# Optimization experiments

Hardware: AMD Instinct MI355X
Metric: run time of the kernel (lower is better)

Reference implementation:

```python
import jax, jax.numpy as jnp
from jax import lax
import numpy as np

B, T, IN, H, L, C = 1024, 64, 64, 512, 8, 128


def setup_inputs() -> dict:
    key = jax.random.key(0)
    ks = jax.random.split(key, 11)
    s_in = 1.0 / np.sqrt(H)
    return {
        "x": jax.random.normal(ks[0], (B, T, IN), jnp.float32),
        "w_ih0": jax.random.normal(ks[1], (4 * H, IN), jnp.float32) * s_in,
        "w_hh0": jax.random.normal(ks[2], (4 * H, H), jnp.float32) * s_in,
        "b_ih0": jax.random.normal(ks[3], (4 * H,), jnp.float32) * s_in,
        "b_hh0": jax.random.normal(ks[4], (4 * H,), jnp.float32) * s_in,
        "w_ih": jax.random.normal(ks[5], (L - 1, 4 * H, H), jnp.float32) * s_in,
        "w_hh": jax.random.normal(ks[6], (L - 1, 4 * H, H), jnp.float32) * s_in,
        "b_ih": jax.random.normal(ks[7], (L - 1, 4 * H), jnp.float32) * s_in,
        "b_hh": jax.random.normal(ks[8], (L - 1, 4 * H), jnp.float32) * s_in,
        "fc_w": jax.random.normal(ks[9], (C, H * T), jnp.float32) * (1.0 / np.sqrt(H * T)),
        "fc_b": jax.random.normal(ks[10], (C,), jnp.float32) * 0.01,
    }


def _lstm_layer(x_tbd, wi, wh, bi, bh):
    # x_tbd: [T, B, D_in]; returns hidden sequence [T, B, H]
    b = x_tbd.shape[1]
    h_dim = wh.shape[1]
    bias = bi + bh

    def step(carry, x_t):
        h, c = carry
        gates = x_t @ wi.T + h @ wh.T + bias  # [B, 4H]
        i, f, g, o = jnp.split(gates, 4, axis=-1)  # PyTorch gate order i,f,g,o
        i = jax.nn.sigmoid(i)
        f = jax.nn.sigmoid(f)
        g = jnp.tanh(g)
        o = jax.nn.sigmoid(o)
        c = f * c + i * g
        h = o * jnp.tanh(c)
        return (h, c), h

    h0 = jnp.zeros((b, h_dim), x_tbd.dtype)
    _, hs = lax.scan(step, (h0, h0), x_tbd)
    return hs


def reference(x, w_ih0, w_hh0, b_ih0, b_hh0, w_ih, w_hh, b_ih, b_hh, fc_w, fc_b):
    xt = jnp.transpose(x, (1, 0, 2))  # [T, B, IN]
    h = _lstm_layer(xt, w_ih0, w_hh0, b_ih0, b_hh0)
    for l in range(w_ih.shape[0]):  # fixed small layer count
        h = _lstm_layer(h, w_ih[l], w_hh[l], b_ih[l], b_hh[l])
    out = jnp.transpose(h, (1, 0, 2)).reshape(x.shape[0], -1)  # [B, T*H]
    return out @ fc_w.T + fc_b
```

## Files before the change

kernel.cpp:

```cpp
#include <hip/hip_runtime.h>
#include <hip/hip_bf16.h>

#define BB   1024
#define TT   64
#define IND  64
#define HH   512
#define G4   2048
#define NLAYER 8
#define NCLS 128
#define KP   1024
#define RS   8
#define SLOT (32 * 1024 * 16)

typedef __bf16 bf16x8 __attribute__((ext_vector_type(8)));
typedef float  f32x4  __attribute__((ext_vector_type(4)));

typedef const __attribute__((address_space(1))) void* as1cvp;
typedef __attribute__((address_space(3))) void* as3vp;

__device__ __forceinline__ void gload16(void* lds, const void* g) {
  __builtin_amdgcn_global_load_lds((as1cvp)g, (as3vp)lds, 16, 0, 0);
}

__device__ __forceinline__ float sigmf(float x) { return 1.f / (1.f + __expf(-x)); }
__device__ __forceinline__ float tanhfast(float x) { return 2.f / (1.f + __expf(-2.f * x)) - 1.f; }

__global__ void cvt_kernel(const float* __restrict__ s, __bf16* __restrict__ d, int n) {
  int i = blockIdx.x * 256 + threadIdx.x;
  if (i < n) d[i] = (__bf16)s[i];
}

__global__ void pack_w(const float* __restrict__ whh0, const float* __restrict__ wih0,
                       const float* __restrict__ whh, const float* __restrict__ wih,
                       __bf16* __restrict__ Wp) {
  int i = blockIdx.x * 256 + threadIdx.x;
  int k = i & (KP - 1), n = (i >> 10) & 2047, l = i >> 21;
  float v;
  if (k < 512) v = (l == 0) ? whh0[n * 512 + k] : whh[((size_t)(l - 1) * G4 + n) * 512 + k];
  else if (l == 0) v = (k < 512 + IND) ? wih0[n * IND + (k - 512)] : 0.f;
  else v = wih[((size_t)(l - 1) * G4 + n) * 512 + (k - 512)];
  Wp[i] = (__bf16)v;
}

__global__ void bias_prep(const float* __restrict__ bi0, const float* __restrict__ bh0,
                          const float* __restrict__ bi, const float* __restrict__ bh,
                          float* __restrict__ biasb) {
  int i = blockIdx.x * 256 + threadIdx.x;
  int l = i >> 11, k = i & 2047;
  float v = (l == 0) ? (bi0[k] + bh0[k]) : (bi[(l - 1) * G4 + k] + bh[(l - 1) * G4 + k]);
  biasb[i] = v;
}

__global__ void zero_u32(unsigned* __restrict__ p, int n) {
  int i = blockIdx.x * 256 + threadIdx.x;
  if (i < n) p[i] = 0u;
}

__global__ __launch_bounds__(256, 2) void lstm_all(
    const float* __restrict__ xf,
    const __bf16* __restrict__ Wp,
    const float* __restrict__ biasb,
    __bf16* __restrict__ hring,
    __bf16* __restrict__ h7,
    unsigned* __restrict__ flags,
    unsigned* __restrict__ xslot) {
  extern __shared__ __bf16 Wlds[];
  __shared__ int sbs;
  const int tid = threadIdx.x;

  if (tid == 0) {
    unsigned xcc;
    asm volatile("s_getreg_b32 %0, hwreg(HW_REG_XCC_ID)" : "=s"(xcc));
    xcc &= 7u;
    unsigned slot = __hip_atomic_fetch_add(xslot + xcc, 1u, __ATOMIC_RELAXED,
                                           __HIP_MEMORY_SCOPE_AGENT) & 63u;
    sbs = (int)((xcc << 6) | slot);
  }
  __syncthreads();
  const int l  = sbs >> 6;
  const int bx = (sbs >> 5) & 1;
  const int by = sbs & 31;
  const int j0 = by << 4;
  const __bf16* Wl = Wp + (size_t)l * G4 * KP;

  for (int it = 0; it < 16; ++it) {
    const int p = it * 256 + tid;
    const int kt = p >> 8;
    const int q = p & 255;
    const int u = q >> 2;
    const int g = (q & 3) ^ ((u >> 1) & 3);
    const int n = ((u >> 4) << 9) + j0 + (u & 15);
    gload16(&Wlds[p * 8], Wl + (size_t)n * KP + kt * 32 + g * 8);
  }

  const int lane = tid & 63, wv = tid >> 6;
  const int qr = lane >> 4, ml = lane & 15;
  const __bf16* wb[4];
  float bv[4];
  int wsw[4];
#pragma unroll
  for (int g = 0; g < 4; ++g) {
    const int n = g * 512 + j0 + ml;
    wb[g] = Wl + (size_t)n * KP + 512 + qr * 8;
    bv[g] = biasb[l * G4 + n];
    const int u = g * 16 + ml;
    wsw[g] = u * 32 + ((qr ^ ((u >> 1) & 3)) << 3);
  }
  const int r0 = (bx << 9) + (wv << 7);
  const int rowA = r0 + ml;
  const int abase = ((qr >> 1) << 14) + rowA * 16 + ((qr & 1) << 3);
  __bf16* ringL = hring + (size_t)l * RS * SLOT;
  const __bf16* ringU = hring + (size_t)((l > 0 ? l : 1) - 1) * RS * SLOT;
  unsigned* ownf = flags + (l * 2 + bx) * 64;
  unsigned* upf  = flags + ((l > 0 ? l - 1 : 0) * 2 + bx) * 64;
  unsigned* dnf  = flags + ((l < 7 ? l + 1 : 7) * 2 + bx) * 64;
  float c8[8][4] = {};
  f32x4 acc[8][4];
  __syncthreads();

  auto initAcc = [&]() {
#pragma unroll
    for (int m = 0; m < 8; ++m)
#pragma unroll
      for (int g = 0; g < 4; ++g)
#pragma unroll
        for (int r = 0; r < 4; ++r) acc[m][g][r] = bv[g];
  };

  auto xpartL0 = [&](int tx) {
#pragma unroll
    for (int m = 0; m < 8; ++m) {
      const float* xr = xf + ((size_t)(rowA + m * 16) * TT + tx) * IND + qr * 8;
      const f32x4 f0 = *(const f32x4*)xr;
      const f32x4 f1 = *(const f32x4*)(xr + 4);
      const f32x4 f2 = *(const f32x4*)(xr + 32);
      const f32x4 f3 = *(const f32x4*)(xr + 36);
      bf16x8 a0, a1;
#pragma unroll
      for (int r = 0; r < 4; ++r) {
        a0[r] = (__bf16)f0[r]; a0[4 + r] = (__bf16)f1[r];
        a1[r] = (__bf16)f2[r]; a1[4 + r] = (__bf16)f3[r];
      }
#pragma unroll
      for (int g = 0; g < 4; ++g) {
        acc[m][g] = __builtin_amdgcn_mfma_f32_16x16x32_bf16(
            a0, *(const bf16x8*)(wb[g]), acc[m][g], 0, 0, 0);
        acc[m][g] = __builtin_amdgcn_mfma_f32_16x16x32_bf16(
            a1, *(const bf16x8*)(wb[g] + 32), acc[m][g], 0, 0, 0);
      }
    }
  };

  auto xpartL = [&](int tx) {
    const __bf16* src = ringU + (size_t)(tx & (RS - 1)) * SLOT + abase;
    bf16x8 A0[4], A1[4], Wr[2][4];
#pragma unroll
    for (int m = 0; m < 4; ++m) A0[m] = *(const bf16x8*)(src + m * 256);
#pragma unroll
    for (int m = 0; m < 4; ++m) A1[m] = *(const bf16x8*)(src + (4 + m) * 256);
#pragma unroll
    for (int g = 0; g < 4; ++g) Wr[0][g] = *(const bf16x8*)(wb[g]);
#pragma unroll
    for (int kt = 0; kt < 16; ++kt) {
      const __bf16* aknx = src + (kt + 1) * 32768;
#pragma unroll
      for (int m = 0; m < 4; ++m)
#pragma unroll
        for (int g = 0; g < 4; ++g)
          acc[m][g] = __builtin_amdgcn_mfma_f32_16x16x32_bf16(
              A0[m], Wr[kt & 1][g], acc[m][g], 0, 0, 0);
      if (kt < 15) {
#pragma unroll
        for (int m = 0; m < 4; ++m) A0[m] = *(const bf16x8*)(aknx + m * 256);
#pragma unroll
        for (int g = 0; g < 4; ++g)
          Wr[(kt + 1) & 1][g] = *(const bf16x8*)(wb[g] + (kt + 1) * 32);
      }
      __builtin_amdgcn_sched_barrier(0);
#pragma unroll
      for (int m = 0; m < 4; ++m)
#pragma unroll
        for (int g = 0; g < 4; ++g)
          acc[4 + m][g] = __builtin_amdgcn_mfma_f32_16x16x32_bf16(
              A1[m], Wr[kt & 1][g], acc[4 + m][g], 0, 0, 0);
      if (kt < 15) {
#pragma unroll
        for (int m = 0; m < 4; ++m) A1[m] = *(const bf16x8*)(aknx + (4 + m) * 256);
      }
      __builtin_amdgcn_sched_barrier(0);
    }
  };

  auto hpart = [&](int t) {
    const __bf16* srcH = ((l < 7) ? ringL + (size_t)((t - 1) & (RS - 1)) * SLOT
                                  : h7 + (size_t)(t - 1) * SLOT) + abase;
    bf16x8 A0[4], A1[4];
#pragma unroll
    for (int m = 0; m < 4; ++m) A0[m] = *(const bf16x8*)(srcH + m * 256);
#pragma unroll
    for (int m = 0; m < 4; ++m) A1[m] = *(const bf16x8*)(srcH + (4 + m) * 256);
#pragma unroll
    for (int kt = 0; kt < 16; ++kt) {
      const __bf16* aknx = srcH + (kt + 1) * 32768;
      bf16x8 wf[4];
#pragma unroll
      for (int g = 0; g < 4; ++g) wf[g] = *(const bf16x8*)&Wlds[kt * 2048 + wsw[g]];
#pragma unroll
      for (int m = 0; m < 4; ++m)
#pragma unroll
        for (int g = 0; g < 4; ++g)
          acc[m][g] = __builtin_amdgcn_mfma_f32_16x16x32_bf16(
              A0[m], wf[g], acc[m][g], 0, 0, 0);
      if (kt < 15) {
#pragma unroll
        for (int m = 0; m < 4; ++m) A0[m] = *(const bf16x8*)(aknx + m * 256);
      }
      __builtin_amdgcn_sched_barrier(0);
#pragma unroll
      for (int m = 0; m < 4; ++m)
#pragma unroll
        for (int g = 0; g < 4; ++g)
          acc[4 + m][g] = __builtin_amdgcn_mfma_f32_16x16x32_bf16(
              A1[m], wf[g], acc[4 + m][g], 0, 0, 0);
      if (kt < 15) {
#pragma unroll
        for (int m = 0; m < 4; ++m) A1[m] = *(const bf16x8*)(aknx + (4 + m) * 256);
      }
      __builtin_amdgcn_sched_barrier(0);
    }
  };

  if (l > 0) {
    if (wv == 0) {
      for (;;) {
        unsigned v = (lane < 32) ? __hip_atomic_load(upf + lane, __ATOMIC_RELAXED,
                                                     __HIP_MEMORY_SCOPE_AGENT)
                                 : 1u;
        if (__all((int)(v >= 1u))) break;
        __builtin_amdgcn_s_sleep(1);
      }
    }
    __syncthreads();
  }
  initAcc();
  if (l == 0) xpartL0(0); else xpartL(0);

  for (int t = 0; t < TT; ++t) {
    if (wv == 0 && t > 0) {
      const unsigned need = (unsigned)t;
      for (;;) {
        unsigned v = (lane < 32) ? __hip_atomic_load(ownf + lane, __ATOMIC_RELAXED,
                                                     __HIP_MEMORY_SCOPE_AGENT)
                                 : need;
        if (__all((int)(v >= need))) break;
        __builtin_amdgcn_s_sleep(1);
      }
    }
    __syncthreads();
    if (t > 0 && (t & (RS - 1)) == 0)
      __builtin_amdgcn_fence(__ATOMIC_ACQUIRE, "agent");

    if (t > 0) hpart(t);

    if (wv == 0 && l < 7 && t >= RS) {
      const unsigned need = (unsigned)(t - (RS - 1));
      for (;;) {
        unsigned v = (lane < 32) ? __hip_atomic_load(dnf + lane, __ATOMIC_RELAXED,
                                                     __HIP_MEMORY_SCOPE_AGENT)
                                 : need;
        if (__all((int)(v >= need))) break;
        __builtin_amdgcn_s_sleep(1);
      }
    }
    __syncthreads();

    unsigned short* dst = (unsigned short*)(((l < 7)
        ? ringL + (size_t)(t & (RS - 1)) * SLOT
        : h7 + (size_t)t * SLOT) + ((size_t)by << 14)) + ml;
#pragma unroll
    for (int m = 0; m < 8; ++m) {
      const int rbm = r0 + m * 16 + (qr << 2);
#pragma unroll
      for (int r = 0; r < 4; ++r) {
        const float gi = sigmf(acc[m][0][r]);
        const float gf = sigmf(acc[m][1][r]);
        const float gg = tanhfast(acc[m][2][r]);
        const float go = sigmf(acc[m][3][r]);
        const float cv = gf * c8[m][r] + gi * gg;
        c8[m][r] = cv;
        const __bf16 hv = (__bf16)(go * tanhfast(cv));
        __hip_atomic_store(dst + (size_t)(rbm + r) * 16,
                           __builtin_bit_cast(unsigned short, hv),
                           __ATOMIC_RELAXED, __HIP_MEMORY_SCOPE_AGENT);
      }
    }
    __syncthreads();
    if (tid == 0)
      __hip_atomic_store(ownf + by, (unsigned)(t + 1), __ATOMIC_RELAXED,
                         __HIP_MEMORY_SCOPE_AGENT);

    if (t + 1 < TT) {
      if (l > 0) {
        if (wv == 0) {
          const unsigned need = (unsigned)(t + 2);
          for (;;) {
            unsigned v = (lane < 32) ? __hip_atomic_load(upf + lane, __ATOMIC_RELAXED,
                                                         __HIP_MEMORY_SCOPE_AGENT)
                                     : need;
            if (__all((int)(v >= need))) break;
            __builtin_amdgcn_s_sleep(1);
          }
        }
        __syncthreads();
      }
      initAcc();
      if (l == 0) xpartL0(t + 1); else xpartL(t + 1);
    }
  }
}

__global__ __launch_bounds__(256, 2) void fc_kernel(
    const __bf16* __restrict__ hseq, const __bf16* __restrict__ fcw,
    float* __restrict__ partial) {
  __shared__ __bf16 At[64 * 32];
  __shared__ __bf16 Wt[128 * 32];
  const int tid = threadIdx.x;
  const int b0 = blockIdx.x * 64;
  const int kbase = blockIdx.y * 2048;
  const int lane = tid & 63, wv = tid >> 6;
  const int qr = lane >> 4, ml = lane & 15;
  const int wr = (wv >> 1) * 32, wc = (wv & 1) * 64;
  const int sr = tid >> 2, sk = (tid & 3) * 8;

  f32x4 acc[2][4];
  for (int i = 0; i < 2; i++)
    for (int j = 0; j < 4; j++)
      for (int r = 0; r < 4; r++) acc[i][j][r] = 0.f;

  for (int kt = 0; kt < 64; ++kt) {
    const int k = kbase + kt * 32;
    const int t = k >> 9;
    const int kk = (k & 511) + sk;
    gload16(&At[tid * 8],
            hseq + (size_t)t * SLOT + ((size_t)(kk >> 4) * 1024 + b0 + sr) * 16 + (kk & 15));
    gload16(&Wt[tid * 8],        fcw + (size_t)sr * (TT * HH) + k + sk);
    gload16(&Wt[2048 + tid * 8], fcw + (size_t)(sr + 64) * (TT * HH) + k + sk);
    __syncthreads();
    bf16x8 af[2], bfr[4];
    for (int i = 0; i < 2; i++) af[i]  = *(const bf16x8*)&At[(wr + i * 16 + ml) * 32 + qr * 8];
    for (int j = 0; j < 4; j++) bfr[j] = *(const bf16x8*)&Wt[(wc + j * 16 + ml) * 32 + qr * 8];
    for (int i = 0; i < 2; i++)
      for (int j = 0; j < 4; j++)
        acc[i][j] = __builtin_amdgcn_mfma_f32_16x16x32_bf16(af[i], bfr[j], acc[i][j], 0, 0, 0);
    __syncthreads();
  }
  for (int i = 0; i < 2; i++)
    for (int j = 0; j < 4; j++)
      for (int r = 0; r < 4; r++)
        partial[((size_t)blockIdx.y * BB + b0 + wr + i * 16 + qr * 4 + r) * NCLS + wc + j * 16 + ml] =
            acc[i][j][r];
}

__global__ void fc_reduce(const float* __restrict__ partial, const float* __restrict__ fcb,
                          float* __restrict__ out) {
  int i = blockIdx.x * 256 + threadIdx.x;
  float s = fcb[i & 127];
  for (int p = 0; p < 16; p++) s += partial[(size_t)p * (BB * NCLS) + i];
  out[i] = s;
}

extern "C" void kernel_launch(void* const* d_in, const int* in_sizes, int n_in,
                              void* d_out, int out_size, void* d_ws, size_t ws_size,
                              hipStream_t stream) {
  const float* x    = (const float*)d_in[0];
  const float* wih0 = (const float*)d_in[1];
  const float* whh0 = (const float*)d_in[2];
  const float* bih0 = (const float*)d_in[3];
  const float* bhh0 = (const float*)d_in[4];
  const float* wih  = (const float*)d_in[5];
  const float* whh  = (const float*)d_in[6];
  const float* bih  = (const float*)d_in[7];
  const float* bhh  = (const float*)d_in[8];
  const float* fcw  = (const float*)d_in[9];
  const float* fcb  = (const float*)d_in[10];
  float* out = (float*)d_out;

  hipFuncSetAttribute((const void*)lstm_all,
                      hipFuncAttributeMaxDynamicSharedMemorySize, 65536);

  size_t off = 0;
  char* base = (char*)d_ws;
  auto carve = [&](size_t bytes) -> char* {
    char* p = base + off;
    off += (bytes + 255) & ~(size_t)255;
    return p;
  };
  __bf16*   Wp    = (__bf16*)carve((size_t)NLAYER * G4 * KP * 2);
  __bf16*   fcwb  = (__bf16*)carve((size_t)NCLS * TT * HH * 2);
  float*    biasb = (float*)carve((size_t)NLAYER * G4 * 4);
  __bf16*   hring = (__bf16*)carve((size_t)7 * RS * SLOT * 2);
  __bf16*   h7    = (__bf16*)carve((size_t)TT * SLOT * 2);
  float*    part  = (float*)carve((size_t)16 * BB * NCLS * 4);
  unsigned* flags = (unsigned*)carve((size_t)(NLAYER * 2 * 64 + 64) * 4);
  unsigned* xslot = flags + NLAYER * 2 * 64;

  pack_w<<<(NLAYER * G4 * KP) / 256, 256, 0, stream>>>(whh0, wih0, whh, wih, Wp);
  cvt_kernel<<<(NCLS * TT * HH) / 256, 256, 0, stream>>>(fcw, fcwb, NCLS * TT * HH);
  bias_prep<<<(NLAYER * G4) / 256, 256, 0, stream>>>(bih0, bhh0, bih, bhh, biasb);
  zero_u32<<<(NLAYER * 2 * 64 + 64 + 255) / 256, 256, 0, stream>>>(
      flags, NLAYER * 2 * 64 + 64);

  lstm_all<<<512, 256, 65536, stream>>>(x, Wp, biasb, hring, h7, flags, xslot);

  fc_kernel<<<dim3(16, 16), 256, 0, stream>>>(h7, fcwb, part);
  fc_reduce<<<(BB * NCLS) / 256, 256, 0, stream>>>(part, fcb, out);
}
```

Before: 3.643 ms.

## Poll upstream layer once and defer input projection instead of spinning

New measurement: 3.870 ms. 6.2% more time.

```diff
diff --git a/kernel.cpp b/kernel.cpp
--- a/kernel.cpp
+++ b/kernel.cpp
@@ -66,6 +66,7 @@
     unsigned* __restrict__ xslot) {
   extern __shared__ __bf16 Wlds[];
   __shared__ int sbs;
+  __shared__ int xdone;
   const int tid = threadIdx.x;
 
   if (tid == 0) {
@@ -153,80 +154,56 @@
 
   auto xpartL = [&](int tx) {
     const __bf16* src = ringU + (size_t)(tx & (RS - 1)) * SLOT + abase;
-    bf16x8 A0[4], A1[4], Wr[2][4];
-#pragma unroll
-    for (int m = 0; m < 4; ++m) A0[m] = *(const bf16x8*)(src + m * 256);
-#pragma unroll
-    for (int m = 0; m < 4; ++m) A1[m] = *(const bf16x8*)(src + (4 + m) * 256);
+    bf16x8 A[8], Wr[2][4];
+#pragma unroll
+    for (int m = 0; m < 8; ++m) A[m] = *(const bf16x8*)(src + m * 256);
 #pragma unroll
     for (int g = 0; g < 4; ++g) Wr[0][g] = *(const bf16x8*)(wb[g]);
 #pragma unroll
     for (int kt = 0; kt < 16; ++kt) {
       const __bf16* aknx = src + (kt + 1) * 32768;
 #pragma unroll
-      for (int m = 0; m < 4; ++m)
+      for (int m = 0; m < 8; ++m) {
 #pragma unroll
         for (int g = 0; g < 4; ++g)
           acc[m][g] = __builtin_amdgcn_mfma_f32_16x16x32_bf16(
-              A0[m], Wr[kt & 1][g], acc[m][g], 0, 0, 0);
-      if (kt < 15) {
-#pragma unroll
-        for (int m = 0; m < 4; ++m) A0[m] = *(const bf16x8*)(aknx + m * 256);
-#pragma unroll
-        for (int g = 0; g < 4; ++g)
-          Wr[(kt + 1) & 1][g] = *(const bf16x8*)(wb[g] + (kt + 1) * 32);
-      }
-      __builtin_amdgcn_sched_barrier(0);
-#pragma unroll
-      for (int m = 0; m < 4; ++m)
-#pragma unroll
-        for (int g = 0; g < 4; ++g)
-          acc[4 + m][g] = __builtin_amdgcn_mfma_f32_16x16x32_bf16(
-              A1[m], Wr[kt & 1][g], acc[4 + m][g], 0, 0, 0);
-      if (kt < 15) {
-#pragma unroll
-        for (int m = 0; m < 4; ++m) A1[m] = *(const bf16x8*)(aknx + (4 + m) * 256);
-      }
-      __builtin_amdgcn_sched_barrier(0);
+              A[m], Wr[kt & 1][g], acc[m][g], 0, 0, 0);
+        if (kt < 15) A[m] = *(const bf16x8*)(aknx + m * 256);
+        if (m == 0 && kt < 15) {
+#pragma unroll
+          for (int g = 0; g < 4; ++g)
+            Wr[(kt + 1) & 1][g] = *(const bf16x8*)(wb[g] + (kt + 1) * 32);
+        }
+        __builtin_amdgcn_sched_barrier(0);
+      }
     }
   };
 
   auto hpart = [&](int t) {
     const __bf16* srcH = ((l < 7) ? ringL + (size_t)((t - 1) & (RS - 1)) * SLOT
                                   : h7 + (size_t)(t - 1) * SLOT) + abase;
-    bf16x8 A0[4], A1[4];
-#pragma unroll
-    for (int m = 0; m < 4; ++m) A0[m] = *(const bf16x8*)(srcH + m * 256);
-#pragma unroll
-    for (int m = 0; m < 4; ++m) A1[m] = *(const bf16x8*)(srcH + (4 + m) * 256);
+    bf16x8 A[8], wf[2][4];
+#pragma unroll
+    for (int m = 0; m < 8; ++m) A[m] = *(const bf16x8*)(srcH + m * 256);
+#pragma unroll
+    for (int g = 0; g < 4; ++g) wf[0][g] = *(const bf16x8*)&Wlds[wsw[g]];
 #pragma unroll
     for (int kt = 0; kt < 16; ++kt) {
       const __bf16* aknx = srcH + (kt + 1) * 32768;
-      bf16x8 wf[4];
-#pragma unroll
-      for (int g = 0; g < 4; ++g) wf[g] = *(const bf16x8*)&Wlds[kt * 2048 + wsw[g]];
-#pragma unroll
-      for (int m = 0; m < 4; ++m)
+#pragma unroll
+      for (int m = 0; m < 8; ++m) {
 #pragma unroll
         for (int g = 0; g < 4; ++g)
           acc[m][g] = __builtin_amdgcn_mfma_f32_16x16x32_bf16(
-              A0[m], wf[g], acc[m][g], 0, 0, 0);
-      if (kt < 15) {
-#pragma unroll
-        for (int m = 0; m < 4; ++m) A0[m] = *(const bf16x8*)(aknx + m * 256);
-      }
-      __builtin_amdgcn_sched_barrier(0);
-#pragma unroll
-      for (int m = 0; m < 4; ++m)
-#pragma unroll
-        for (int g = 0; g < 4; ++g)
-          acc[4 + m][g] = __builtin_amdgcn_mfma_f32_16x16x32_bf16(
-              A1[m], wf[g], acc[4 + m][g], 0, 0, 0);
-      if (kt < 15) {
-#pragma unroll
-        for (int m = 0; m < 4; ++m) A1[m] = *(const bf16x8*)(aknx + (4 + m) * 256);
-      }
-      __builtin_amdgcn_sched_barrier(0);
+              A[m], wf[kt & 1][g], acc[m][g], 0, 0, 0);
+        if (kt < 15) A[m] = *(const bf16x8*)(aknx + m * 256);
+        if (m == 4 && kt < 15) {
+#pragma unroll
+          for (int g = 0; g < 4; ++g)
+            wf[(kt + 1) & 1][g] = *(const bf16x8*)&Wlds[(kt + 1) * 2048 + wsw[g]];
+        }
+        __builtin_amdgcn_sched_barrier(0);
+      }
     }
   };
 
@@ -244,6 +221,7 @@
   }
   initAcc();
   if (l == 0) xpartL0(0); else xpartL(0);
+  bool have_x = true;
 
   for (int t = 0; t < TT; ++t) {
     if (wv == 0 && t > 0) {
@@ -259,6 +237,24 @@
     __syncthreads();
     if (t > 0 && (t & (RS - 1)) == 0)
       __builtin_amdgcn_fence(__ATOMIC_ACQUIRE, "agent");
+
+    if (!have_x) {
+      if (l > 0) {
+        if (wv == 0) {
+          const unsigned need = (unsigned)(t + 1);
+          for (;;) {
+            unsigned v = (lane < 32) ? __hip_atomic_load(upf + lane, __ATOMIC_RELAXED,
+                                                         __HIP_MEMORY_SCOPE_AGENT)
+                                     : need;
+            if (__all((int)(v >= need))) break;
+            __builtin_amdgcn_s_sleep(1);
+          }
+        }
+        __syncthreads();
+      }
+      initAcc();
+      if (l == 0) xpartL0(t); else xpartL(t);
+    }
 
     if (t > 0) hpart(t);
 
@@ -300,21 +296,30 @@
                          __HIP_MEMORY_SCOPE_AGENT);
 
     if (t + 1 < TT) {
-      if (l > 0) {
+      if (l == 0) {
+        initAcc();
+        xpartL0(t + 1);
+        have_x = true;
+      } else {
         if (wv == 0) {
           const unsigned need = (unsigned)(t + 2);
-          for (;;) {
-            unsigned v = (lane < 32) ? __hip_atomic_load(upf + lane, __ATOMIC_RELAXED,
-                                                         __HIP_MEMORY_SCOPE_AGENT)
-                                     : need;
-            if (__all((int)(v >= need))) break;
-            __builtin_amdgcn_s_sleep(1);
-          }
+          unsigned v = (lane < 32) ? __hip_atomic_load(upf + lane, __ATOMIC_RELAXED,
+                                                       __HIP_MEMORY_SCOPE_AGENT)
+                                   : need;
+          const int ok = __all((int)(v >= need)) ? 1 : 0;
+          if (lane == 0) xdone = ok;
         }
         __syncthreads();
-      }
-      initAcc();
-      if (l == 0) xpartL0(t + 1); else xpartL(t + 1);
+        if (xdone) {
+          if (((t + 1) & (RS - 1)) == 0)
+            __builtin_amdgcn_fence(__ATOMIC_ACQUIRE, "agent");
+          initAcc();
+          xpartL(t + 1);
+          have_x = true;
+        } else {
+          have_x = false;
+        }
+      }
     }
   }
 }
```
